# Kernel optimization log

Measured on AMD Instinct MI355X. Metric: run time of the kernel, lower is better.

Reference implementation:

```python
import jax, jax.numpy as jnp
import numpy as np


def setup_inputs() -> dict:
    key = jax.random.key(0)
    k1, k2, k3, k4, k5 = jax.random.split(key, 5)
    N, T, D, H = 256, 64, 1024, 1024
    x = jax.random.normal(k1, (N, T, D), dtype=jnp.float32)
    A = jax.random.normal(k2, (N, H, 4, 4), dtype=jnp.float32)
    Wx = jax.random.normal(k3, (D, 4 * H), dtype=jnp.float32) / np.sqrt(D)
    Wh = jax.random.normal(k4, (H, 4 * H), dtype=jnp.float32) / np.sqrt(H)
    Wattn = jax.random.normal(k5, (H, 4 * H), dtype=jnp.float32) / np.sqrt(H)
    b = jnp.zeros((4 * H,), dtype=jnp.float32)
    return {"x": x, "A": A, "Wx": Wx, "Wh": Wh, "Wattn": Wattn, "b": b}


def reference(x, A, Wx, Wh, Wattn, b):
    N, T, D = x.shape
    H = A.shape[1]
    A_flat = A.reshape(N, H, 16)           # (N, H, 16) flattened 4x4 grid
    scale = 1.0 / jnp.sqrt(jnp.asarray(H, dtype=x.dtype))

    h0 = A.mean(axis=(2, 3))               # (N, H)
    c0 = h0

    def step(carry, xt):
        prev_h, prev_c = carry
        # scaled dot-product attention over the 16 spatial locations
        scores = jnp.einsum('nh,nhl->nl', prev_h, A_flat) * scale  # (N, 16)
        w = jax.nn.softmax(scores, axis=1)
        attn = jnp.einsum('nhl,nl->nh', A_flat, w)                 # (N, H)
        # fused LSTM gate pre-activation
        a = xt @ Wx + prev_h @ Wh + attn @ Wattn + b               # (N, 4H)
        ai, af, ao, ag = jnp.split(a, 4, axis=1)
        i = jax.nn.sigmoid(ai)
        f = jax.nn.sigmoid(af)
        o = jax.nn.sigmoid(ao)
        g = jnp.tanh(ag)
        next_c = f * prev_c + i * g
        next_h = o * jnp.tanh(next_c)
        return (next_h, next_c), next_h

    xs = jnp.swapaxes(x, 0, 1)             # (T, N, D)
    _, hs = jax.lax.scan(step, (h0, c0), xs)
    return jnp.swapaxes(hs, 0, 1)          # (N, T, H)
```

## Files before the change

kernel.cpp:

```cpp
#include <hip/hip_runtime.h>

typedef _Float16 f16;
typedef _Float16 f16x4 __attribute__((ext_vector_type(4)));
typedef _Float16 f16x8 __attribute__((ext_vector_type(8)));
typedef float f32x4 __attribute__((ext_vector_type(4)));

#define N_ 256
#define T_ 64
#define D_ 1024
#define H_ 1024
#define K3 3072
#define G4 4096

__global__ void k_transpose(const float* __restrict__ Wx, const float* __restrict__ Wh,
                            const float* __restrict__ Wattn, f16* __restrict__ W3T) {
    __shared__ float tile[32][33];
    int j0 = blockIdx.x * 32;
    int k0 = blockIdx.y * 32;
    int tx = threadIdx.x;
    int ty = threadIdx.y;
    for (int i = 0; i < 4; i++) {
        int k = k0 + ty + i * 8;
        const float* W = (k < 1024) ? Wx : ((k < 2048) ? Wh : Wattn);
        int kr = k & 1023;
        tile[ty + i * 8][tx] = W[(size_t)kr * 4096 + j0 + tx];
    }
    __syncthreads();
    for (int i = 0; i < 4; i++) {
        int j = j0 + ty + i * 8;
        W3T[(size_t)j * K3 + k0 + tx] = (f16)tile[tx][ty + i * 8];
    }
}

__global__ void k_castA(const float* __restrict__ A, f16* __restrict__ A16) {
    int i = blockIdx.x * 256 + threadIdx.x;
    float4 v = ((const float4*)A)[i];
    f16x4 h4 = {(f16)v.x, (f16)v.y, (f16)v.z, (f16)v.w};
    ((f16x4*)A16)[i] = h4;
}

__global__ void k_castX(const float* __restrict__ x, f16* __restrict__ x16) {
    size_t i = (size_t)blockIdx.x * 2048 + (size_t)threadIdx.x * 8;
    float4 v0 = *(const float4*)(x + i);
    float4 v1 = *(const float4*)(x + i + 4);
    f16x8 h;
    h[0] = (f16)v0.x; h[1] = (f16)v0.y; h[2] = (f16)v0.z; h[3] = (f16)v0.w;
    h[4] = (f16)v1.x; h[5] = (f16)v1.y; h[6] = (f16)v1.z; h[7] = (f16)v1.w;
    *(f16x8*)(x16 + i) = h;
}

__global__ void k_init(const float* __restrict__ A, f16* __restrict__ Zh,
                       float* __restrict__ c, float* __restrict__ spart) {
    int n = blockIdx.x;
    int tid = threadIdx.x;
    __shared__ float sred[256][16];
    float s[16];
#pragma unroll
    for (int l = 0; l < 16; l++) s[l] = 0.f;
    for (int i = 0; i < 4; i++) {
        int h = tid + i * 256;
        const float* Ap = A + (size_t)n * 16384 + h * 16;
        float a[16];
        float sum = 0.f;
#pragma unroll
        for (int l = 0; l < 16; l++) { a[l] = Ap[l]; sum += a[l]; }
        float h0 = sum * (1.f / 16.f);
        c[n * 1024 + h] = h0;
        Zh[n * 1024 + h] = (f16)h0;
#pragma unroll
        for (int l = 0; l < 16; l++) s[l] += h0 * a[l];
    }
#pragma unroll
    for (int l = 0; l < 16; l++) sred[tid][l] = s[l];
    __syncthreads();
    for (int st = 128; st > 0; st >>= 1) {
        if (tid < st) {
#pragma unroll
            for (int l = 0; l < 16; l++) sred[tid][l] += sred[tid + st][l];
        }
        __syncthreads();
    }
    if (tid < 16) spart[(size_t)n * 16 + tid] = sred[0][tid];
    for (int i = 0; i < 4; i++) {
        int idx = tid * 4 + i;
        if (idx < 1008) {
            int ht = 1 + (idx >> 4);
            int l = idx & 15;
            spart[((size_t)ht * 256 + n) * 16 + l] = 0.f;
        }
    }
}

__global__ void k_attn(const float* __restrict__ spart, const f16* __restrict__ A16,
                       f16* __restrict__ Za) {
    int n = blockIdx.x;
    int tid = threadIdx.x;
    __shared__ float sred[16][17];
    __shared__ float sfin[16];
    int g = tid >> 4;
    int l = tid & 15;
    float p = 0.f;
#pragma unroll
    for (int i = 0; i < 4; i++) {
        int ht = g + i * 16;
        p += spart[((size_t)ht * 256 + n) * 16 + l];
    }
    sred[g][l] = p;
    __syncthreads();
    if (tid < 16) {
        float s = 0.f;
#pragma unroll
        for (int gg = 0; gg < 16; gg++) s += sred[gg][tid];
        sfin[tid] = s;
    }
    __syncthreads();
    float w[16];
    float mx = -1e30f;
#pragma unroll
    for (int ll = 0; ll < 16; ll++) { w[ll] = sfin[ll] * 0.03125f; mx = fmaxf(mx, w[ll]); }
    float sum = 0.f;
#pragma unroll
    for (int ll = 0; ll < 16; ll++) { w[ll] = __expf(w[ll] - mx); sum += w[ll]; }
    float inv = 1.f / sum;
#pragma unroll
    for (int ll = 0; ll < 16; ll++) w[ll] *= inv;
    for (int i = 0; i < 4; i++) {
        int h = tid * 4 + i;
        const f16* Ap = A16 + (size_t)n * 16384 + h * 16;
        f16x8 a0 = *(const f16x8*)(Ap);
        f16x8 a1 = *(const f16x8*)(Ap + 8);
        float acc = 0.f;
#pragma unroll
        for (int ll = 0; ll < 8; ll++) acc += (float)a0[ll] * w[ll] + (float)a1[ll] * w[ll + 8];
        Za[n * 1024 + h] = (f16)acc;
    }
}

__global__ __launch_bounds__(512, 2) void k_step(
    const f16* __restrict__ x16, const f16* __restrict__ W3T,
    const f16* __restrict__ Zin, f16* __restrict__ Zout,
    const f16* __restrict__ Za, const f16* __restrict__ A16,
    const float* __restrict__ b, float* __restrict__ c,
    float* __restrict__ spart, float* __restrict__ out, int t) {
    __shared__ float Gs[4][4][64 * 17];
    __shared__ float Hs[64 * 17];

    int tid = threadIdx.x;
    int wave = tid >> 6;
    int lane = tid & 63;
    int m16 = lane & 15;
    int quad = lane >> 4;
    int bid = blockIdx.x;
    int ht = bid & 63;
    int n0 = (bid >> 6) << 6;
    int hc = ht * 16;

    f32x4 acc[4][4];
#pragma unroll
    for (int g = 0; g < 4; g++)
#pragma unroll
        for (int m = 0; m < 4; m++) acc[g][m] = (f32x4){0.f, 0.f, 0.f, 0.f};

    const f16* brow[4];
#pragma unroll
    for (int g = 0; g < 4; g++)
        brow[g] = W3T + (size_t)(g * 1024 + hc + m16) * K3 + quad * 8;

    size_t offx[4], offz[4];
#pragma unroll
    for (int mt = 0; mt < 4; mt++) {
        int n = n0 + mt * 16 + m16;
        offx[mt] = (size_t)n * (T_ * 1024);
        offz[mt] = (size_t)n * 1024;
    }
    const f16* xbase = x16 + (size_t)t * 1024 + quad * 8;
    const f16* zbase0 = Zin + quad * 8;
    const f16* zbase1 = Za + quad * 8;

    int kbase = wave * 384;
#pragma unroll 2
    for (int s = 0; s < 12; s++) {
        int k = kbase + s * 32;
        int seg = k >> 10;
        int kk = k & 1023;
        const f16* base;
        const size_t* off;
        if (seg == 0)      { base = xbase;  off = offx; }
        else if (seg == 1) { base = zbase0; off = offz; }
        else               { base = zbase1; off = offz; }
        f16x8 a[4], bb[4];
#pragma unroll
        for (int mt = 0; mt < 4; mt++) a[mt] = *(const f16x8*)(base + off[mt] + kk);
#pragma unroll
        for (int g = 0; g < 4; g++) bb[g] = *(const f16x8*)(brow[g] + k);
#pragma unroll
        for (int g = 0; g < 4; g++)
#pragma unroll
            for (int mt = 0; mt < 4; mt++)
                acc[g][mt] = __builtin_amdgcn_mfma_f32_16x16x32_f16(a[mt], bb[g], acc[g][mt], 0, 0, 0);
    }

    if (wave < 4) {
#pragma unroll
        for (int g = 0; g < 4; g++)
#pragma unroll
            for (int mt = 0; mt < 4; mt++)
#pragma unroll
                for (int r = 0; r < 4; r++)
                    Gs[wave][g][(mt * 16 + quad * 4 + r) * 17 + m16] = acc[g][mt][r];
    }
    __syncthreads();
    if (wave >= 4) {
        int sl = wave - 4;
#pragma unroll
        for (int g = 0; g < 4; g++)
#pragma unroll
            for (int mt = 0; mt < 4; mt++)
#pragma unroll
                for (int r = 0; r < 4; r++)
                    Gs[sl][g][(mt * 16 + quad * 4 + r) * 17 + m16] += acc[g][mt][r];
    }
    __syncthreads();

    for (int i = 0; i < 2; i++) {
        int idx = i * 512 + tid;
        int nn = idx >> 4;
        int hh = idx & 15;
        int gi = nn * 17 + hh;
        int gn = n0 + nn;
        int gh = hc + hh;
        float ai = Gs[0][0][gi] + Gs[1][0][gi] + Gs[2][0][gi] + Gs[3][0][gi] + b[gh];
        float af = Gs[0][1][gi] + Gs[1][1][gi] + Gs[2][1][gi] + Gs[3][1][gi] + b[1024 + gh];
        float ao = Gs[0][2][gi] + Gs[1][2][gi] + Gs[2][2][gi] + Gs[3][2][gi] + b[2048 + gh];
        float ag = Gs[0][3][gi] + Gs[1][3][gi] + Gs[2][3][gi] + Gs[3][3][gi] + b[3072 + gh];
        float ig = 1.f / (1.f + __expf(-ai));
        float fg = 1.f / (1.f + __expf(-af));
        float og = 1.f / (1.f + __expf(-ao));
        float gg = tanhf(ag);
        float cn = fg * c[gn * 1024 + gh] + ig * gg;
        c[gn * 1024 + gh] = cn;
        float hn = og * tanhf(cn);
        out[((size_t)gn * T_ + t) * 1024 + gh] = hn;
        Zout[gn * 1024 + gh] = (f16)hn;
        Hs[gi] = hn;
    }
    __syncthreads();

    for (int i = 0; i < 2; i++) {
        int idx = i * 512 + tid;
        int nn = idx >> 4;
        int l = idx & 15;
        int gn = n0 + nn;
        const f16* Ap = A16 + (size_t)gn * 16384 + hc * 16 + l;
        float s = 0.f;
#pragma unroll
        for (int hh = 0; hh < 16; hh++)
            s += Hs[nn * 17 + hh] * (float)Ap[hh * 16];
        spart[((size_t)ht * 256 + gn) * 16 + l] = s;
    }
}

extern "C" void kernel_launch(void* const* d_in, const int* in_sizes, int n_in,
                              void* d_out, int out_size, void* d_ws, size_t ws_size,
                              hipStream_t stream) {
    const float* x     = (const float*)d_in[0];
    const float* A     = (const float*)d_in[1];
    const float* Wx    = (const float*)d_in[2];
    const float* Wh    = (const float*)d_in[3];
    const float* Wattn = (const float*)d_in[4];
    const float* b     = (const float*)d_in[5];
    float* out = (float*)d_out;

    char* ws = (char*)d_ws;
    size_t off = 0;
    f16* W3T = (f16*)(ws + off); off += (size_t)G4 * K3 * 2;
    f16* x16 = (f16*)(ws + off); off += (size_t)N_ * T_ * D_ * 2;
    f16* A16 = (f16*)(ws + off); off += (size_t)N_ * H_ * 16 * 2;
    f16* Zh0 = (f16*)(ws + off); off += (size_t)N_ * H_ * 2;
    f16* Zh1 = (f16*)(ws + off); off += (size_t)N_ * H_ * 2;
    f16* Za  = (f16*)(ws + off); off += (size_t)N_ * H_ * 2;
    float* c = (float*)(ws + off); off += (size_t)N_ * H_ * 4;
    float* spart = (float*)(ws + off); off += (size_t)64 * N_ * 16 * 4;

    k_transpose<<<dim3(128, 96), dim3(32, 8), 0, stream>>>(Wx, Wh, Wattn, W3T);
    k_castA<<<4096, 256, 0, stream>>>(A, A16);
    k_castX<<<8192, 256, 0, stream>>>(x, x16);
    k_init<<<256, 256, 0, stream>>>(A, Zh0, c, spart);
    for (int t = 0; t < T_; t++) {
        f16* Zin  = (t & 1) ? Zh1 : Zh0;
        f16* Zout = (t & 1) ? Zh0 : Zh1;
        k_attn<<<256, 256, 0, stream>>>(spart, A16, Za);
        k_step<<<256, 512, 0, stream>>>(x16, W3T, Zin, Zout, Za, A16, b, c, spart, out, t);
    }
}
```

Baseline: 2.244 ms.

## Fuse per-step attention and LSTM kernels into one persistent kernel with grid barriers

Replaces the 128 per-timestep launches of k_attn and k_step with a single persistent kernel of 256 blocks that loops over timesteps. Blocks synchronise through a software grid barrier built on atomic counters. The attention step is folded into each block, and the x and h parts of the gate GEMM run before waiting on the attention barrier, so that work overlaps the wait. It relies on all 256 blocks being co-resident, and adds spin-wait cost plus a risk of deadlock if they are not.

```diff
diff --git a/kernel.cpp b/kernel.cpp
--- a/kernel.cpp
+++ b/kernel.cpp
@@ -1,6 +1,7 @@
 #include <hip/hip_runtime.h>
 
 typedef _Float16 f16;
+typedef _Float16 f16x2 __attribute__((ext_vector_type(2)));
 typedef _Float16 f16x4 __attribute__((ext_vector_type(4)));
 typedef _Float16 f16x8 __attribute__((ext_vector_type(8)));
 typedef float f32x4 __attribute__((ext_vector_type(4)));
@@ -11,6 +12,7 @@
 #define H_ 1024
 #define K3 3072
 #define G4 4096
+#define NBLK 256
 
 __global__ void k_transpose(const float* __restrict__ Wx, const float* __restrict__ Wh,
                             const float* __restrict__ Wattn, f16* __restrict__ W3T) {
@@ -50,9 +52,11 @@
 }
 
 __global__ void k_init(const float* __restrict__ A, f16* __restrict__ Zh,
-                       float* __restrict__ c, float* __restrict__ spart) {
+                       float* __restrict__ c, float* __restrict__ spart,
+                       int* __restrict__ bar) {
     int n = blockIdx.x;
     int tid = threadIdx.x;
+    if (n == 0 && tid == 0) { bar[0] = 0; bar[32] = 0; }
     __shared__ float sred[256][16];
     float s[16];
 #pragma unroll
@@ -91,59 +95,17 @@
     }
 }
 
-__global__ void k_attn(const float* __restrict__ spart, const f16* __restrict__ A16,
-                       f16* __restrict__ Za) {
-    int n = blockIdx.x;
-    int tid = threadIdx.x;
-    __shared__ float sred[16][17];
-    __shared__ float sfin[16];
-    int g = tid >> 4;
-    int l = tid & 15;
-    float p = 0.f;
-#pragma unroll
-    for (int i = 0; i < 4; i++) {
-        int ht = g + i * 16;
-        p += spart[((size_t)ht * 256 + n) * 16 + l];
-    }
-    sred[g][l] = p;
-    __syncthreads();
-    if (tid < 16) {
-        float s = 0.f;
-#pragma unroll
-        for (int gg = 0; gg < 16; gg++) s += sred[gg][tid];
-        sfin[tid] = s;
-    }
-    __syncthreads();
-    float w[16];
-    float mx = -1e30f;
-#pragma unroll
-    for (int ll = 0; ll < 16; ll++) { w[ll] = sfin[ll] * 0.03125f; mx = fmaxf(mx, w[ll]); }
-    float sum = 0.f;
-#pragma unroll
-    for (int ll = 0; ll < 16; ll++) { w[ll] = __expf(w[ll] - mx); sum += w[ll]; }
-    float inv = 1.f / sum;
-#pragma unroll
-    for (int ll = 0; ll < 16; ll++) w[ll] *= inv;
-    for (int i = 0; i < 4; i++) {
-        int h = tid * 4 + i;
-        const f16* Ap = A16 + (size_t)n * 16384 + h * 16;
-        f16x8 a0 = *(const f16x8*)(Ap);
-        f16x8 a1 = *(const f16x8*)(Ap + 8);
-        float acc = 0.f;
-#pragma unroll
-        for (int ll = 0; ll < 8; ll++) acc += (float)a0[ll] * w[ll] + (float)a1[ll] * w[ll + 8];
-        Za[n * 1024 + h] = (f16)acc;
-    }
-}
-
-__global__ __launch_bounds__(512, 2) void k_step(
+__global__ __launch_bounds__(512, 2) void k_persist(
     const f16* __restrict__ x16, const f16* __restrict__ W3T,
-    const f16* __restrict__ Zin, f16* __restrict__ Zout,
-    const f16* __restrict__ Za, const f16* __restrict__ A16,
+    f16* __restrict__ Zh0, f16* __restrict__ Zh1,
+    f16* __restrict__ Za, const f16* __restrict__ A16,
     const float* __restrict__ b, float* __restrict__ c,
-    float* __restrict__ spart, float* __restrict__ out, int t) {
+    float* __restrict__ spart, float* __restrict__ out,
+    int* bar) {
     __shared__ float Gs[4][4][64 * 17];
     __shared__ float Hs[64 * 17];
+    __shared__ float sredA[32][17];
+    __shared__ float sfinA[16];
 
     int tid = threadIdx.x;
     int wave = tid >> 6;
@@ -154,12 +116,9 @@
     int ht = bid & 63;
     int n0 = (bid >> 6) << 6;
     int hc = ht * 16;
-
-    f32x4 acc[4][4];
-#pragma unroll
-    for (int g = 0; g < 4; g++)
-#pragma unroll
-        for (int m = 0; m < 4; m++) acc[g][m] = (f32x4){0.f, 0.f, 0.f, 0.f};
+    int* cnt = bar;
+    int* gen = bar + 32;
+    int bgen = 0;
 
     const f16* brow[4];
 #pragma unroll
@@ -173,90 +132,195 @@
         offx[mt] = (size_t)n * (T_ * 1024);
         offz[mt] = (size_t)n * 1024;
     }
-    const f16* xbase = x16 + (size_t)t * 1024 + quad * 8;
-    const f16* zbase0 = Zin + quad * 8;
-    const f16* zbase1 = Za + quad * 8;
-
-    int kbase = wave * 384;
+    int kb = wave * 128;
+
+    for (int t = 0; t < T_; t++) {
+        const f16* Zin = (t & 1) ? Zh1 : Zh0;
+        f16* Zout = (t & 1) ? Zh0 : Zh1;
+
+        {
+            int ga = tid >> 4;
+            int l = tid & 15;
+            sredA[ga][l] = spart[((size_t)ga * 256 + bid) * 16 + l]
+                         + spart[((size_t)(ga + 32) * 256 + bid) * 16 + l];
+        }
+        __syncthreads();
+        if (tid < 16) {
+            float s = 0.f;
+#pragma unroll
+            for (int gg = 0; gg < 32; gg++) s += sredA[gg][tid];
+            sfinA[tid] = s;
+        }
+        __syncthreads();
+        {
+            float w[16];
+            float mx = -1e30f;
+#pragma unroll
+            for (int ll = 0; ll < 16; ll++) { w[ll] = sfinA[ll] * 0.03125f; mx = fmaxf(mx, w[ll]); }
+            float sum = 0.f;
+#pragma unroll
+            for (int ll = 0; ll < 16; ll++) { w[ll] = __expf(w[ll] - mx); sum += w[ll]; }
+            float inv = 1.f / sum;
+            const f16* Ap = A16 + (size_t)bid * 16384 + (size_t)tid * 32;
+            f16x2 za2;
+#pragma unroll
+            for (int i = 0; i < 2; i++) {
+                f16x8 a0 = *(const f16x8*)(Ap + i * 16);
+                f16x8 a1 = *(const f16x8*)(Ap + i * 16 + 8);
+                float acc = 0.f;
+#pragma unroll
+                for (int ll = 0; ll < 8; ll++)
+                    acc += (float)a0[ll] * w[ll] + (float)a1[ll] * w[ll + 8];
+                za2[i] = (f16)(acc * inv);
+            }
+            *(f16x2*)(Za + bid * 1024 + tid * 2) = za2;
+        }
+
+        __syncthreads();
+        if (tid == 0) {
+            __builtin_amdgcn_fence(__ATOMIC_RELEASE, "agent");
+            int old = __hip_atomic_fetch_add(cnt, 1, __ATOMIC_RELAXED, __HIP_MEMORY_SCOPE_AGENT);
+            if (old == NBLK - 1) {
+                __hip_atomic_store(cnt, 0, __ATOMIC_RELAXED, __HIP_MEMORY_SCOPE_AGENT);
+                __hip_atomic_store(gen, bgen + 1, __ATOMIC_RELEASE, __HIP_MEMORY_SCOPE_AGENT);
+            }
+        }
+
+        f32x4 acc[4][4];
+#pragma unroll
+        for (int g = 0; g < 4; g++)
+#pragma unroll
+            for (int m = 0; m < 4; m++) acc[g][m] = (f32x4){0.f, 0.f, 0.f, 0.f};
+
+        const f16* xb = x16 + (size_t)t * 1024 + kb + quad * 8;
+        const f16* hb = Zin + kb + quad * 8;
+        const f16* ab = Za + kb + quad * 8;
+
 #pragma unroll 2
-    for (int s = 0; s < 12; s++) {
-        int k = kbase + s * 32;
-        int seg = k >> 10;
-        int kk = k & 1023;
-        const f16* base;
-        const size_t* off;
-        if (seg == 0)      { base = xbase;  off = offx; }
-        else if (seg == 1) { base = zbase0; off = offz; }
-        else               { base = zbase1; off = offz; }
-        f16x8 a[4], bb[4];
-#pragma unroll
-        for (int mt = 0; mt < 4; mt++) a[mt] = *(const f16x8*)(base + off[mt] + kk);
-#pragma unroll
-        for (int g = 0; g < 4; g++) bb[g] = *(const f16x8*)(brow[g] + k);
-#pragma unroll
-        for (int g = 0; g < 4; g++)
-#pragma unroll
-            for (int mt = 0; mt < 4; mt++)
-                acc[g][mt] = __builtin_amdgcn_mfma_f32_16x16x32_f16(a[mt], bb[g], acc[g][mt], 0, 0, 0);
-    }
-
-    if (wave < 4) {
-#pragma unroll
-        for (int g = 0; g < 4; g++)
-#pragma unroll
-            for (int mt = 0; mt < 4; mt++)
-#pragma unroll
-                for (int r = 0; r < 4; r++)
-                    Gs[wave][g][(mt * 16 + quad * 4 + r) * 17 + m16] = acc[g][mt][r];
-    }
-    __syncthreads();
-    if (wave >= 4) {
-        int sl = wave - 4;
-#pragma unroll
-        for (int g = 0; g < 4; g++)
-#pragma unroll
-            for (int mt = 0; mt < 4; mt++)
-#pragma unroll
-                for (int r = 0; r < 4; r++)
-                    Gs[sl][g][(mt * 16 + quad * 4 + r) * 17 + m16] += acc[g][mt][r];
-    }
-    __syncthreads();
-
-    for (int i = 0; i < 2; i++) {
-        int idx = i * 512 + tid;
-        int nn = idx >> 4;
-        int hh = idx & 15;
-        int gi = nn * 17 + hh;
-        int gn = n0 + nn;
-        int gh = hc + hh;
-        float ai = Gs[0][0][gi] + Gs[1][0][gi] + Gs[2][0][gi] + Gs[3][0][gi] + b[gh];
-        float af = Gs[0][1][gi] + Gs[1][1][gi] + Gs[2][1][gi] + Gs[3][1][gi] + b[1024 + gh];
-        float ao = Gs[0][2][gi] + Gs[1][2][gi] + Gs[2][2][gi] + Gs[3][2][gi] + b[2048 + gh];
-        float ag = Gs[0][3][gi] + Gs[1][3][gi] + Gs[2][3][gi] + Gs[3][3][gi] + b[3072 + gh];
-        float ig = 1.f / (1.f + __expf(-ai));
-        float fg = 1.f / (1.f + __expf(-af));
-        float og = 1.f / (1.f + __expf(-ao));
-        float gg = tanhf(ag);
-        float cn = fg * c[gn * 1024 + gh] + ig * gg;
-        c[gn * 1024 + gh] = cn;
-        float hn = og * tanhf(cn);
-        out[((size_t)gn * T_ + t) * 1024 + gh] = hn;
-        Zout[gn * 1024 + gh] = (f16)hn;
-        Hs[gi] = hn;
-    }
-    __syncthreads();
-
-    for (int i = 0; i < 2; i++) {
-        int idx = i * 512 + tid;
-        int nn = idx >> 4;
-        int l = idx & 15;
-        int gn = n0 + nn;
-        const f16* Ap = A16 + (size_t)gn * 16384 + hc * 16 + l;
-        float s = 0.f;
-#pragma unroll
-        for (int hh = 0; hh < 16; hh++)
-            s += Hs[nn * 17 + hh] * (float)Ap[hh * 16];
-        spart[((size_t)ht * 256 + gn) * 16 + l] = s;
+        for (int j = 0; j < 4; j++) {
+            int k = j * 32;
+            f16x8 a[4], bb[4];
+#pragma unroll
+            for (int mt = 0; mt < 4; mt++) a[mt] = *(const f16x8*)(xb + offx[mt] + k);
+#pragma unroll
+            for (int g = 0; g < 4; g++) bb[g] = *(const f16x8*)(brow[g] + kb + k);
+#pragma unroll
+            for (int g = 0; g < 4; g++)
+#pragma unroll
+                for (int mt = 0; mt < 4; mt++)
+                    acc[g][mt] = __builtin_amdgcn_mfma_f32_16x16x32_f16(a[mt], bb[g], acc[g][mt], 0, 0, 0);
+        }
+#pragma unroll 2
+        for (int j = 0; j < 4; j++) {
+            int k = j * 32;
+            f16x8 a[4], bb[4];
+#pragma unroll
+            for (int mt = 0; mt < 4; mt++) a[mt] = *(const f16x8*)(hb + offz[mt] + k);
+#pragma unroll
+            for (int g = 0; g < 4; g++) bb[g] = *(const f16x8*)(brow[g] + 1024 + kb + k);
+#pragma unroll
+            for (int g = 0; g < 4; g++)
+#pragma unroll
+                for (int mt = 0; mt < 4; mt++)
+                    acc[g][mt] = __builtin_amdgcn_mfma_f32_16x16x32_f16(a[mt], bb[g], acc[g][mt], 0, 0, 0);
+        }
+
+        while (__hip_atomic_load(gen, __ATOMIC_RELAXED, __HIP_MEMORY_SCOPE_AGENT) == bgen)
+            __builtin_amdgcn_s_sleep(1);
+        __builtin_amdgcn_fence(__ATOMIC_ACQUIRE, "agent");
+        bgen++;
+
+#pragma unroll 2
+        for (int j = 0; j < 4; j++) {
+            int k = j * 32;
+            f16x8 a[4], bb[4];
+#pragma unroll
+            for (int mt = 0; mt < 4; mt++) a[mt] = *(const f16x8*)(ab + offz[mt] + k);
+#pragma unroll
+            for (int g = 0; g < 4; g++) bb[g] = *(const f16x8*)(brow[g] + 2048 + kb + k);
+#pragma unroll
+            for (int g = 0; g < 4; g++)
+#pragma unroll
+                for (int mt = 0; mt < 4; mt++)
+                    acc[g][mt] = __builtin_amdgcn_mfma_f32_16x16x32_f16(a[mt], bb[g], acc[g][mt], 0, 0, 0);
+        }
+
+        if (wave < 4) {
+#pragma unroll
+            for (int g = 0; g < 4; g++)
+#pragma unroll
+                for (int mt = 0; mt < 4; mt++)
+#pragma unroll
+                    for (int r = 0; r < 4; r++)
+                        Gs[wave][g][(mt * 16 + quad * 4 + r) * 17 + m16] = acc[g][mt][r];
+        }
+        __syncthreads();
+        if (wave >= 4) {
+            int sl = wave - 4;
+#pragma unroll
+            for (int g = 0; g < 4; g++)
+#pragma unroll
+                for (int mt = 0; mt < 4; mt++)
+#pragma unroll
+                    for (int r = 0; r < 4; r++)
+                        Gs[sl][g][(mt * 16 + quad * 4 + r) * 17 + m16] += acc[g][mt][r];
+        }
+        __syncthreads();
+
+#pragma unroll
+        for (int i = 0; i < 2; i++) {
+            int idx = i * 512 + tid;
+            int nn = idx >> 4;
+            int hh = idx & 15;
+            int gi = nn * 17 + hh;
+            int gn = n0 + nn;
+            int gh = hc + hh;
+            float ai = Gs[0][0][gi] + Gs[1][0][gi] + Gs[2][0][gi] + Gs[3][0][gi] + b[gh];
+            float af = Gs[0][1][gi] + Gs[1][1][gi] + Gs[2][1][gi] + Gs[3][1][gi] + b[1024 + gh];
+            float ao = Gs[0][2][gi] + Gs[1][2][gi] + Gs[2][2][gi] + Gs[3][2][gi] + b[2048 + gh];
+            float ag = Gs[0][3][gi] + Gs[1][3][gi] + Gs[2][3][gi] + Gs[3][3][gi] + b[3072 + gh];
+            float ig = 1.f / (1.f + __expf(-ai));
+            float fg = 1.f / (1.f + __expf(-af));
+            float og = 1.f / (1.f + __expf(-ao));
+            float gg = tanhf(ag);
+            float cn = fg * c[gn * 1024 + gh] + ig * gg;
+            c[gn * 1024 + gh] = cn;
+            float hn = og * tanhf(cn);
+            out[((size_t)gn * T_ + t) * 1024 + gh] = hn;
+            Zout[gn * 1024 + gh] = (f16)hn;
+            Hs[gi] = hn;
+        }
+        __syncthreads();
+
+#pragma unroll
+        for (int i = 0; i < 2; i++) {
+            int idx = i * 512 + tid;
+            int nn = idx >> 4;
+            int l = idx & 15;
+            int gn = n0 + nn;
+            const f16* Ap = A16 + (size_t)gn * 16384 + hc * 16 + l;
+            float s = 0.f;
+#pragma unroll
+            for (int hh = 0; hh < 16; hh++)
+                s += Hs[nn * 17 + hh] * (float)Ap[hh * 16];
+            spart[((size_t)ht * 256 + gn) * 16 + l] = s;
+        }
+
+        __syncthreads();
+        if (tid == 0) {
+            __builtin_amdgcn_fence(__ATOMIC_RELEASE, "agent");
+            int old = __hip_atomic_fetch_add(cnt, 1, __ATOMIC_RELAXED, __HIP_MEMORY_SCOPE_AGENT);
+            if (old == NBLK - 1) {
+                __hip_atomic_store(cnt, 0, __ATOMIC_RELAXED, __HIP_MEMORY_SCOPE_AGENT);
+                __hip_atomic_store(gen, bgen + 1, __ATOMIC_RELEASE, __HIP_MEMORY_SCOPE_AGENT);
+            } else {
+                while (__hip_atomic_load(gen, __ATOMIC_RELAXED, __HIP_MEMORY_SCOPE_AGENT) == bgen)
+                    __builtin_amdgcn_s_sleep(2);
+            }
+            __builtin_amdgcn_fence(__ATOMIC_ACQUIRE, "agent");
+        }
+        __syncthreads();
+        bgen++;
     }
 }
 
@@ -281,15 +345,11 @@
     f16* Za  = (f16*)(ws + off); off += (size_t)N_ * H_ * 2;
     float* c = (float*)(ws + off); off += (size_t)N_ * H_ * 4;
     float* spart = (float*)(ws + off); off += (size_t)64 * N_ * 16 * 4;
+    int* bar = (int*)(ws + off); off += 256;
 
     k_transpose<<<dim3(128, 96), dim3(32, 8), 0, stream>>>(Wx, Wh, Wattn, W3T);
     k_castA<<<4096, 256, 0, stream>>>(A, A16);
     k_castX<<<8192, 256, 0, stream>>>(x, x16);
-    k_init<<<256, 256, 0, stream>>>(A, Zh0, c, spart);
-    for (int t = 0; t < T_; t++) {
-        f16* Zin  = (t & 1) ? Zh1 : Zh0;
-        f16* Zout = (t & 1) ? Zh0 : Zh1;
-        k_attn<<<256, 256, 0, stream>>>(spart, A16, Za);
-        k_step<<<256, 512, 0, stream>>>(x16, W3T, Zin, Zout, Za, A16, b, c, spart, out, t);
-    }
-}
+    k_init<<<256, 256, 0, stream>>>(A, Zh0, c, spart, bar);
+    k_persist<<<256, 512, 0, stream>>>(x16, W3T, Zh0, Zh1, Za, A16, b, c, spart, out, bar);
+}
```

Result: slower. 3.832 ms (+70.8%).

## Precompute A·Wattn projection and fold softmax attention into LSTM step kernel

Applied to the files above, without the earlier changes.

Reassociates attn@Wattn as softmax weights times a precomputed per-batch projection P = A^T·Wattn (N×4H×16), computed once before the recurrence. The per-step GEMM shrinks from K=3072 to K=2048, and the separate attention kernel disappears: the softmax runs inside the step kernel, and score partials are accumulated with atomics into a triple-rotated buffer. It adds a large precompute (about 256 small GEMMs) and a 32MB PT16 buffer that every step reads, plus the fp16 rounding of P.

```diff
diff --git a/kernel.cpp b/kernel.cpp
--- a/kernel.cpp
+++ b/kernel.cpp
@@ -1,6 +1,7 @@
 #include <hip/hip_runtime.h>
 
 typedef _Float16 f16;
+typedef _Float16 f16x2 __attribute__((ext_vector_type(2)));
 typedef _Float16 f16x4 __attribute__((ext_vector_type(4)));
 typedef _Float16 f16x8 __attribute__((ext_vector_type(8)));
 typedef float f32x4 __attribute__((ext_vector_type(4)));
@@ -49,8 +50,69 @@
     *(f16x8*)(x16 + i) = h;
 }
 
+__global__ void k_castAT(const float* __restrict__ A, f16* __restrict__ AT16) {
+    __shared__ f16 sA[16 * 1024];
+    int n = blockIdx.x;
+    int tid = threadIdx.x;
+    for (int i = 0; i < 4; i++) {
+        int h = tid + i * 256;
+        const float* Ap = A + (size_t)n * 16384 + h * 16;
+        float4 v0 = ((const float4*)Ap)[0];
+        float4 v1 = ((const float4*)Ap)[1];
+        float4 v2 = ((const float4*)Ap)[2];
+        float4 v3 = ((const float4*)Ap)[3];
+        float vv[16] = {v0.x, v0.y, v0.z, v0.w, v1.x, v1.y, v1.z, v1.w,
+                        v2.x, v2.y, v2.z, v2.w, v3.x, v3.y, v3.z, v3.w};
+#pragma unroll
+        for (int l = 0; l < 16; l++) sA[l * 1024 + h] = (f16)vv[l];
+    }
+    __syncthreads();
+    for (int i = 0; i < 8; i++) {
+        int cnk = tid + i * 256;
+        f16x8 v = *(const f16x8*)(sA + cnk * 8);
+        *(f16x8*)(AT16 + (size_t)n * 16384 + cnk * 8) = v;
+    }
+}
+
+__global__ __launch_bounds__(512) void k_precompP(
+    const f16* __restrict__ AT16, const f16* __restrict__ W3T,
+    f16* __restrict__ PT16) {
+    int tid = threadIdx.x;
+    int wave = tid >> 6;
+    int lane = tid & 63;
+    int m16 = lane & 15;
+    int quad = lane >> 4;
+    int bid = blockIdx.x;
+    int jb = bid & 31;
+    int nb = bid >> 5;
+    int j0 = jb * 128 + wave * 16;
+
+    const f16* bp = W3T + (size_t)(j0 + m16) * K3 + 2048 + quad * 8;
+    for (int np = 0; np < 16; np++) {
+        int n = nb * 32 + np * 2;
+        const f16* a0p = AT16 + (size_t)n * 16384 + m16 * 1024 + quad * 8;
+        const f16* a1p = a0p + 16384;
+        f32x4 ac0 = {0.f, 0.f, 0.f, 0.f};
+        f32x4 ac1 = {0.f, 0.f, 0.f, 0.f};
+#pragma unroll 4
+        for (int ks = 0; ks < 32; ks++) {
+            int k = ks * 32;
+            f16x8 bb = *(const f16x8*)(bp + k);
+            f16x8 a0 = *(const f16x8*)(a0p + k);
+            f16x8 a1 = *(const f16x8*)(a1p + k);
+            ac0 = __builtin_amdgcn_mfma_f32_16x16x32_f16(a0, bb, ac0, 0, 0, 0);
+            ac1 = __builtin_amdgcn_mfma_f32_16x16x32_f16(a1, bb, ac1, 0, 0, 0);
+        }
+        f16x4 o0 = {(f16)ac0[0], (f16)ac0[1], (f16)ac0[2], (f16)ac0[3]};
+        f16x4 o1 = {(f16)ac1[0], (f16)ac1[1], (f16)ac1[2], (f16)ac1[3]};
+        *(f16x4*)(PT16 + (size_t)n * 65536 + (size_t)(j0 + m16) * 16 + quad * 4) = o0;
+        *(f16x4*)(PT16 + (size_t)(n + 1) * 65536 + (size_t)(j0 + m16) * 16 + quad * 4) = o1;
+    }
+}
+
 __global__ void k_init(const float* __restrict__ A, f16* __restrict__ Zh,
-                       float* __restrict__ c, float* __restrict__ spart) {
+                       float* __restrict__ c, float* __restrict__ Sc0,
+                       float* __restrict__ Sc1, float* __restrict__ Sc2) {
     int n = blockIdx.x;
     int tid = threadIdx.x;
     __shared__ float sred[256][16];
@@ -80,70 +142,23 @@
         }
         __syncthreads();
     }
-    if (tid < 16) spart[(size_t)n * 16 + tid] = sred[0][tid];
-    for (int i = 0; i < 4; i++) {
-        int idx = tid * 4 + i;
-        if (idx < 1008) {
-            int ht = 1 + (idx >> 4);
-            int l = idx & 15;
-            spart[((size_t)ht * 256 + n) * 16 + l] = 0.f;
-        }
-    }
-}
-
-__global__ void k_attn(const float* __restrict__ spart, const f16* __restrict__ A16,
-                       f16* __restrict__ Za) {
-    int n = blockIdx.x;
-    int tid = threadIdx.x;
-    __shared__ float sred[16][17];
-    __shared__ float sfin[16];
-    int g = tid >> 4;
-    int l = tid & 15;
-    float p = 0.f;
-#pragma unroll
-    for (int i = 0; i < 4; i++) {
-        int ht = g + i * 16;
-        p += spart[((size_t)ht * 256 + n) * 16 + l];
-    }
-    sred[g][l] = p;
-    __syncthreads();
     if (tid < 16) {
-        float s = 0.f;
-#pragma unroll
-        for (int gg = 0; gg < 16; gg++) s += sred[gg][tid];
-        sfin[tid] = s;
-    }
-    __syncthreads();
-    float w[16];
-    float mx = -1e30f;
-#pragma unroll
-    for (int ll = 0; ll < 16; ll++) { w[ll] = sfin[ll] * 0.03125f; mx = fmaxf(mx, w[ll]); }
-    float sum = 0.f;
-#pragma unroll
-    for (int ll = 0; ll < 16; ll++) { w[ll] = __expf(w[ll] - mx); sum += w[ll]; }
-    float inv = 1.f / sum;
-#pragma unroll
-    for (int ll = 0; ll < 16; ll++) w[ll] *= inv;
-    for (int i = 0; i < 4; i++) {
-        int h = tid * 4 + i;
-        const f16* Ap = A16 + (size_t)n * 16384 + h * 16;
-        f16x8 a0 = *(const f16x8*)(Ap);
-        f16x8 a1 = *(const f16x8*)(Ap + 8);
-        float acc = 0.f;
-#pragma unroll
-        for (int ll = 0; ll < 8; ll++) acc += (float)a0[ll] * w[ll] + (float)a1[ll] * w[ll + 8];
-        Za[n * 1024 + h] = (f16)acc;
+        Sc0[n * 16 + tid] = sred[0][tid];
+        Sc1[n * 16 + tid] = 0.f;
+        Sc2[n * 16 + tid] = 0.f;
     }
 }
 
 __global__ __launch_bounds__(512, 2) void k_step(
     const f16* __restrict__ x16, const f16* __restrict__ W3T,
     const f16* __restrict__ Zin, f16* __restrict__ Zout,
-    const f16* __restrict__ Za, const f16* __restrict__ A16,
+    const f16* __restrict__ A16, const f16* __restrict__ PT16,
     const float* __restrict__ b, float* __restrict__ c,
-    float* __restrict__ spart, float* __restrict__ out, int t) {
+    const float* __restrict__ Rbuf, float* __restrict__ Wbuf,
+    float* __restrict__ Zbuf, float* __restrict__ out, int t) {
     __shared__ float Gs[4][4][64 * 17];
     __shared__ float Hs[64 * 17];
+    __shared__ float Ws[64][17];
 
     int tid = threadIdx.x;
     int wave = tid >> 6;
@@ -155,42 +170,60 @@
     int n0 = (bid >> 6) << 6;
     int hc = ht * 16;
 
+    if (tid < 64) {
+        const float* rp = Rbuf + (size_t)(n0 + tid) * 16;
+        float4 q0 = ((const float4*)rp)[0];
+        float4 q1 = ((const float4*)rp)[1];
+        float4 q2 = ((const float4*)rp)[2];
+        float4 q3 = ((const float4*)rp)[3];
+        float v[16] = {q0.x, q0.y, q0.z, q0.w, q1.x, q1.y, q1.z, q1.w,
+                       q2.x, q2.y, q2.z, q2.w, q3.x, q3.y, q3.z, q3.w};
+        float mx = -1e30f;
+#pragma unroll
+        for (int l = 0; l < 16; l++) { v[l] *= 0.03125f; mx = fmaxf(mx, v[l]); }
+        float sum = 0.f;
+#pragma unroll
+        for (int l = 0; l < 16; l++) { v[l] = __expf(v[l] - mx); sum += v[l]; }
+        float inv = 1.f / sum;
+#pragma unroll
+        for (int l = 0; l < 16; l++) Ws[tid][l] = v[l] * inv;
+    }
+    if (tid < 16) Zbuf[bid * 16 + tid] = 0.f;
+
     f32x4 acc[4][4];
 #pragma unroll
     for (int g = 0; g < 4; g++)
 #pragma unroll
         for (int m = 0; m < 4; m++) acc[g][m] = (f32x4){0.f, 0.f, 0.f, 0.f};
 
+    int kb = (wave & 3) * 256;
+    const f16* ab;
+    size_t aoff[4];
+    int bc0;
+    if (wave < 4) {
+        ab = x16 + (size_t)t * 1024 + kb + quad * 8;
+#pragma unroll
+        for (int mt = 0; mt < 4; mt++)
+            aoff[mt] = (size_t)(n0 + mt * 16 + m16) * (T_ * 1024);
+        bc0 = kb;
+    } else {
+        ab = Zin + kb + quad * 8;
+#pragma unroll
+        for (int mt = 0; mt < 4; mt++)
+            aoff[mt] = (size_t)(n0 + mt * 16 + m16) * 1024;
+        bc0 = 1024 + kb;
+    }
     const f16* brow[4];
 #pragma unroll
     for (int g = 0; g < 4; g++)
-        brow[g] = W3T + (size_t)(g * 1024 + hc + m16) * K3 + quad * 8;
-
-    size_t offx[4], offz[4];
-#pragma unroll
-    for (int mt = 0; mt < 4; mt++) {
-        int n = n0 + mt * 16 + m16;
-        offx[mt] = (size_t)n * (T_ * 1024);
-        offz[mt] = (size_t)n * 1024;
-    }
-    const f16* xbase = x16 + (size_t)t * 1024 + quad * 8;
-    const f16* zbase0 = Zin + quad * 8;
-    const f16* zbase1 = Za + quad * 8;
-
-    int kbase = wave * 384;
+        brow[g] = W3T + (size_t)(g * 1024 + hc + m16) * K3 + bc0 + quad * 8;
+
 #pragma unroll 2
-    for (int s = 0; s < 12; s++) {
-        int k = kbase + s * 32;
-        int seg = k >> 10;
-        int kk = k & 1023;
-        const f16* base;
-        const size_t* off;
-        if (seg == 0)      { base = xbase;  off = offx; }
-        else if (seg == 1) { base = zbase0; off = offz; }
-        else               { base = zbase1; off = offz; }
+    for (int s = 0; s < 8; s++) {
+        int k = s * 32;
         f16x8 a[4], bb[4];
 #pragma unroll
-        for (int mt = 0; mt < 4; mt++) a[mt] = *(const f16x8*)(base + off[mt] + kk);
+        for (int mt = 0; mt < 4; mt++) a[mt] = *(const f16x8*)(ab + aoff[mt] + k);
 #pragma unroll
         for (int g = 0; g < 4; g++) bb[g] = *(const f16x8*)(brow[g] + k);
 #pragma unroll
@@ -222,30 +255,57 @@
     }
     __syncthreads();
 
-    for (int i = 0; i < 2; i++) {
-        int idx = i * 512 + tid;
-        int nn = idx >> 4;
-        int hh = idx & 15;
-        int gi = nn * 17 + hh;
+    {
+        int idx0 = tid * 2;
+        int nn = idx0 >> 4;
+        int hh0 = idx0 & 15;
         int gn = n0 + nn;
-        int gh = hc + hh;
-        float ai = Gs[0][0][gi] + Gs[1][0][gi] + Gs[2][0][gi] + Gs[3][0][gi] + b[gh];
-        float af = Gs[0][1][gi] + Gs[1][1][gi] + Gs[2][1][gi] + Gs[3][1][gi] + b[1024 + gh];
-        float ao = Gs[0][2][gi] + Gs[1][2][gi] + Gs[2][2][gi] + Gs[3][2][gi] + b[2048 + gh];
-        float ag = Gs[0][3][gi] + Gs[1][3][gi] + Gs[2][3][gi] + Gs[3][3][gi] + b[3072 + gh];
-        float ig = 1.f / (1.f + __expf(-ai));
-        float fg = 1.f / (1.f + __expf(-af));
-        float og = 1.f / (1.f + __expf(-ao));
-        float gg = tanhf(ag);
-        float cn = fg * c[gn * 1024 + gh] + ig * gg;
-        c[gn * 1024 + gh] = cn;
-        float hn = og * tanhf(cn);
-        out[((size_t)gn * T_ + t) * 1024 + gh] = hn;
-        Zout[gn * 1024 + gh] = (f16)hn;
-        Hs[gi] = hn;
-    }
-    __syncthreads();
-
+        int gh0 = hc + hh0;
+        float wv[16];
+#pragma unroll
+        for (int l = 0; l < 16; l++) wv[l] = Ws[nn][l];
+        float att[4][2];
+        const f16* pt = PT16 + (size_t)gn * 65536 + (size_t)gh0 * 16;
+#pragma unroll
+        for (int g = 0; g < 4; g++)
+#pragma unroll
+            for (int i = 0; i < 2; i++) {
+                const f16* p = pt + ((size_t)g * 1024 + i) * 16;
+                f16x8 p0 = *(const f16x8*)(p);
+                f16x8 p1 = *(const f16x8*)(p + 8);
+                float s = 0.f;
+#pragma unroll
+                for (int l = 0; l < 8; l++)
+                    s += (float)p0[l] * wv[l] + (float)p1[l] * wv[l + 8];
+                att[g][i] = s;
+            }
+        float hn2[2];
+#pragma unroll
+        for (int i = 0; i < 2; i++) {
+            int gi = nn * 17 + hh0 + i;
+            int gh = gh0 + i;
+            float ai = Gs[0][0][gi] + Gs[1][0][gi] + Gs[2][0][gi] + Gs[3][0][gi] + b[gh] + att[0][i];
+            float af = Gs[0][1][gi] + Gs[1][1][gi] + Gs[2][1][gi] + Gs[3][1][gi] + b[1024 + gh] + att[1][i];
+            float ao = Gs[0][2][gi] + Gs[1][2][gi] + Gs[2][2][gi] + Gs[3][2][gi] + b[2048 + gh] + att[2][i];
+            float ag = Gs[0][3][gi] + Gs[1][3][gi] + Gs[2][3][gi] + Gs[3][3][gi] + b[3072 + gh] + att[3][i];
+            float ig = 1.f / (1.f + __expf(-ai));
+            float fg = 1.f / (1.f + __expf(-af));
+            float og = 1.f / (1.f + __expf(-ao));
+            float gg = tanhf(ag);
+            float cn = fg * c[gn * 1024 + gh] + ig * gg;
+            c[gn * 1024 + gh] = cn;
+            float hn = og * tanhf(cn);
+            hn2[i] = hn;
+            Hs[gi] = hn;
+        }
+        float2 o2 = {hn2[0], hn2[1]};
+        *(float2*)(out + ((size_t)gn * T_ + t) * 1024 + gh0) = o2;
+        f16x2 z2 = {(f16)hn2[0], (f16)hn2[1]};
+        *(f16x2*)(Zout + gn * 1024 + gh0) = z2;
+    }
+    __syncthreads();
+
+#pragma unroll
     for (int i = 0; i < 2; i++) {
         int idx = i * 512 + tid;
         int nn = idx >> 4;
@@ -256,7 +316,7 @@
 #pragma unroll
         for (int hh = 0; hh < 16; hh++)
             s += Hs[nn * 17 + hh] * (float)Ap[hh * 16];
-        spart[((size_t)ht * 256 + gn) * 16 + l] = s;
+        atomicAdd(Wbuf + gn * 16 + l, s);
     }
 }
 
@@ -273,23 +333,30 @@
 
     char* ws = (char*)d_ws;
     size_t off = 0;
-    f16* W3T = (f16*)(ws + off); off += (size_t)G4 * K3 * 2;
-    f16* x16 = (f16*)(ws + off); off += (size_t)N_ * T_ * D_ * 2;
-    f16* A16 = (f16*)(ws + off); off += (size_t)N_ * H_ * 16 * 2;
-    f16* Zh0 = (f16*)(ws + off); off += (size_t)N_ * H_ * 2;
-    f16* Zh1 = (f16*)(ws + off); off += (size_t)N_ * H_ * 2;
-    f16* Za  = (f16*)(ws + off); off += (size_t)N_ * H_ * 2;
-    float* c = (float*)(ws + off); off += (size_t)N_ * H_ * 4;
-    float* spart = (float*)(ws + off); off += (size_t)64 * N_ * 16 * 4;
+    f16* W3T  = (f16*)(ws + off); off += (size_t)G4 * K3 * 2;
+    f16* x16  = (f16*)(ws + off); off += (size_t)N_ * T_ * D_ * 2;
+    f16* A16  = (f16*)(ws + off); off += (size_t)N_ * H_ * 16 * 2;
+    f16* AT16 = (f16*)(ws + off); off += (size_t)N_ * 16 * H_ * 2;
+    f16* PT16 = (f16*)(ws + off); off += (size_t)N_ * G4 * 16 * 2;
+    f16* Zh0  = (f16*)(ws + off); off += (size_t)N_ * H_ * 2;
+    f16* Zh1  = (f16*)(ws + off); off += (size_t)N_ * H_ * 2;
+    float* c  = (float*)(ws + off); off += (size_t)N_ * H_ * 4;
+    float* Sc0 = (float*)(ws + off); off += (size_t)N_ * 16 * 4;
+    float* Sc1 = (float*)(ws + off); off += (size_t)N_ * 16 * 4;
+    float* Sc2 = (float*)(ws + off); off += (size_t)N_ * 16 * 4;
+    float* Sc[3] = {Sc0, Sc1, Sc2};
 
     k_transpose<<<dim3(128, 96), dim3(32, 8), 0, stream>>>(Wx, Wh, Wattn, W3T);
     k_castA<<<4096, 256, 0, stream>>>(A, A16);
     k_castX<<<8192, 256, 0, stream>>>(x, x16);
-    k_init<<<256, 256, 0, stream>>>(A, Zh0, c, spart);
+    k_castAT<<<256, 256, 0, stream>>>(A, AT16);
+    k_precompP<<<256, 512, 0, stream>>>(AT16, W3T, PT16);
+    k_init<<<256, 256, 0, stream>>>(A, Zh0, c, Sc0, Sc1, Sc2);
     for (int t = 0; t < T_; t++) {
         f16* Zin  = (t & 1) ? Zh1 : Zh0;
         f16* Zout = (t & 1) ? Zh0 : Zh1;
-        k_attn<<<256, 256, 0, stream>>>(spart, A16, Za);
-        k_step<<<256, 512, 0, stream>>>(x16, W3T, Zin, Zout, Za, A16, b, c, spart, out, t);
-    }
-}
+        k_step<<<256, 512, 0, stream>>>(x16, W3T, Zin, Zout, A16, PT16, b, c,
+                                        Sc[t % 3], Sc[(t + 1) % 3], Sc[(t + 2) % 3],
+                                        out, t);
+    }
+}
```

After: 2.327 ms. +3.7%, slower.
